# Kernel optimization log

Measured on AMD Instinct MI355X. Metric: run time of the kernel, lower is better.

## Reference

```python
import jax, jax.numpy as jnp
import numpy as np

WS = 8          # window size
DIM = 512       # channels
NH = 16         # heads
HD = DIM // NH  # head dim = 32
N = WS * WS     # tokens per window = 64
NW = 64         # windows per image
B = 16          # images
BW = B * NW     # total windows = 1024
SCALE = HD ** -0.5


def _relative_position_index():
    # Swin relative position index, shape (N, N), values in [0, (2*WS-1)^2)
    coords = np.stack(np.meshgrid(np.arange(WS), np.arange(WS), indexing='ij'))  # (2, WS, WS)
    coords_flat = coords.reshape(2, -1)                                           # (2, N)
    rel = coords_flat[:, :, None] - coords_flat[:, None, :]                       # (2, N, N)
    rel = rel.transpose(1, 2, 0).astype(np.int32)                                 # (N, N, 2)
    rel[:, :, 0] += WS - 1
    rel[:, :, 1] += WS - 1
    rel[:, :, 0] *= 2 * WS - 1
    return jnp.asarray(rel.sum(-1))                                               # (N, N)


def setup_inputs() -> dict:
    key = jax.random.key(0)
    ks = jax.random.split(key, 7)
    x = jax.random.normal(ks[0], (BW, N, DIM), dtype=jnp.float32)
    mask = jax.random.normal(ks[1], (NW, N, N), dtype=jnp.float32)  # shift mask (additive)
    qkv_w = jax.random.normal(ks[2], (3 * DIM, DIM), dtype=jnp.float32) * 0.02
    qkv_b = jax.random.normal(ks[3], (3 * DIM,), dtype=jnp.float32) * 0.02
    rel_bias_table = jax.random.normal(ks[4], ((2 * WS - 1) ** 2, NH), dtype=jnp.float32) * 0.02
    proj_w = jax.random.normal(ks[5], (DIM, DIM), dtype=jnp.float32) * 0.02
    proj_b = jax.random.normal(ks[6], (DIM,), dtype=jnp.float32) * 0.02
    rel_index = _relative_position_index()
    return {"x": x, "mask": mask, "qkv_w": qkv_w, "qkv_b": qkv_b,
            "rel_bias_table": rel_bias_table, "proj_w": proj_w, "proj_b": proj_b,
            "rel_index": rel_index}


def reference(x, mask, qkv_w, qkv_b, rel_bias_table, proj_w, proj_b, rel_index):
    # qkv projection: (BW, N, 3*DIM) -> (3, BW, NH, N, HD)
    qkv = (x @ qkv_w.T + qkv_b).reshape(BW, N, 3, NH, HD).transpose(2, 0, 3, 1, 4)
    q, k, v = qkv[0], qkv[1], qkv[2]
    # scaled dot-product scores: (BW, NH, N, N)
    attn = jnp.einsum('bhnd,bhmd->bhnm', q * SCALE, k)
    # relative position bias: gather (N*N,) -> (N, N, NH) -> (NH, N, N)
    bias = rel_bias_table[rel_index.reshape(-1)].reshape(N, N, NH).transpose(2, 0, 1)
    attn = attn + bias[None]
    # shift mask: broadcast over images and heads
    attn = attn.reshape(B, NW, NH, N, N) + mask[None, :, None]
    attn = jax.nn.softmax(attn.reshape(BW, NH, N, N), axis=-1)
    # weighted values: (BW, NH, N, HD) -> (BW, N, DIM)
    out = jnp.einsum('bhnm,bhmd->bhnd', attn, v).transpose(0, 2, 1, 3).reshape(BW, N, DIM)
    return out @ proj_w.T + proj_b
```

## Files before the change

kernel.cpp:

```cpp
#include <hip/hip_runtime.h>
#include <hip/hip_bf16.h>

typedef __bf16 bf16;
typedef __bf16 bf16x4 __attribute__((ext_vector_type(4)));
typedef __bf16 bf16x8 __attribute__((ext_vector_type(8)));
typedef float  f32x4  __attribute__((ext_vector_type(4)));

#define AS1 __attribute__((address_space(1)))
#define AS3 __attribute__((address_space(3)))

__device__ __forceinline__ void gld_lds16(const void* g, void* l) {
    __builtin_amdgcn_global_load_lds((AS1 void*)g, (AS3 void*)l, 16, 0, 0);
}

__global__ void cvt_kernel(const float* __restrict__ in, bf16* __restrict__ out,
                           int n4) {
    for (long i = (long)blockIdx.x * blockDim.x + threadIdx.x; i < n4;
         i += (long)gridDim.x * blockDim.x) {
        f32x4 v = ((const f32x4*)in)[i];
        bf16x4 h;
#pragma unroll
        for (int e = 0; e < 4; ++e) h[e] = (bf16)v[e];
        ((bf16x4*)out)[i] = h;
    }
}

__global__ void bias_kernel(const int* __restrict__ rel_index,
                            const float* __restrict__ table,
                            float* __restrict__ bias) {
    int idx = blockIdx.x * 256 + threadIdx.x;
    int rc = idx & 4095;
    int h  = idx >> 12;
    bias[idx] = table[rel_index[rc] * 16 + h];
}

#define STAGE(GBASE, LBASE, SK0)                                          \
    { _Pragma("unroll")                                                   \
      for (int c_ = 0; c_ < 2; ++c_)                                      \
          gld_lds16((GBASE) + c_ * 16 * 512 + (SK0),                      \
                    (LBASE) + (w * 2 + c_) * 512); }

#define PHASE(S, KK, IH, LOADB, GB, LB, SK0, VM)                            \
  {                                                                         \
    const bf16* ap_ = sA + ((S)*2+(KK))*8192 + (wm128+(IH)*64+r16)*32 + q*8;\
    _Pragma("unroll")                                                       \
    for (int ii = 0; ii < 4; ++ii) av[ii] = *(const bf16x8*)(ap_ + ii*512); \
    if (LOADB) {                                                            \
      const bf16* bp_ = sB + ((S)*2+(KK))*8192 + (wn64+r16)*32 + q*8;       \
      _Pragma("unroll")                                                     \
      for (int jj = 0; jj < 4; ++jj) bv[jj] = *(const bf16x8*)(bp_+jj*512); \
    }                                                                       \
    STAGE(GB, LB, SK0);                                                     \
    __builtin_amdgcn_sched_barrier(0);                                      \
    __builtin_amdgcn_s_barrier();                                           \
    asm volatile("s_waitcnt lgkmcnt(0)");                                   \
    __builtin_amdgcn_sched_barrier(0);                                      \
    __builtin_amdgcn_s_setprio(1);                                          \
    _Pragma("unroll")                                                       \
    for (int ii = 0; ii < 4; ++ii)                                          \
      _Pragma("unroll")                                                     \
      for (int jj = 0; jj < 4; ++jj)                                        \
        acc[(IH)*4+ii][jj] = __builtin_amdgcn_mfma_f32_16x16x32_bf16(       \
            av[ii], bv[jj], acc[(IH)*4+ii][jj], 0, 0, 0);                   \
    __builtin_amdgcn_s_setprio(0);                                          \
    if (VM) asm volatile("s_waitcnt vmcnt(4)");                             \
    __builtin_amdgcn_sched_barrier(0);                                      \
    __builtin_amdgcn_s_barrier();                                           \
  }

__global__ __launch_bounds__(512, 2) void gemm1_qkv8(
    const bf16* __restrict__ A, const bf16* __restrict__ B,
    const float* __restrict__ bias, bf16* __restrict__ Cq,
    bf16* __restrict__ Ckv)
{
    __shared__ __attribute__((aligned(16))) char smemraw[131072];
    bf16* sA = (bf16*)smemraw;
    bf16* sB = sA + 32768;

    const int t     = threadIdx.x;
    const int w     = t >> 6;
    const int lane  = t & 63;
    const int q     = lane >> 4;
    const int r16   = lane & 15;
    const int wm128 = (w >> 2) * 128;
    const int wn64  = (w & 3) * 64;

    const int bid = blockIdx.x;
    const int wg  = (bid & 7) * 192 + (bid >> 3);
    const long bM = (long)(wg / 6) * 256;
    const long bN = (long)(wg % 6) * 256;

    const bf16* Ast = A + (bM + w * 32 + (lane >> 2)) * 512 + (lane & 3) * 8;
    const bf16* Bst = B + (bN + w * 32 + (lane >> 2)) * 512 + (lane & 3) * 8;

    f32x4 acc[8][4];
#pragma unroll
    for (int i = 0; i < 8; ++i)
#pragma unroll
        for (int j = 0; j < 4; ++j) acc[i][j] = f32x4{0.f, 0.f, 0.f, 0.f};

    bf16x8 av[4], bv[4];

    STAGE(Ast, sA + 0,     0);
    STAGE(Bst, sB + 0,     0);
    STAGE(Ast, sA + 8192,  32);
    STAGE(Bst, sB + 8192,  32);
    STAGE(Ast, sA + 16384, 64);
    STAGE(Bst, sB + 16384, 64);
    asm volatile("s_waitcnt vmcnt(4)");
    __builtin_amdgcn_sched_barrier(0);
    __builtin_amdgcn_s_barrier();

    for (int i = 0; i < 4; ++i) {
        const int t1 = 2 * i + 1;
        const int t2 = (2 * i + 2 < 8) ? 2 * i + 2 : 7;
        const int t3 = (2 * i + 3 < 8) ? 2 * i + 3 : 7;
        PHASE(0, 0, 0, 1, Ast, sA + 24576, t1 * 64 + 32, 0)
        PHASE(0, 0, 1, 0, Bst, sB + 24576, t1 * 64 + 32, 0)
        PHASE(0, 1, 1, 1, Ast, sA + 0,     t2 * 64,      0)
        PHASE(0, 1, 0, 0, Bst, sB + 0,     t2 * 64,      1)
        PHASE(1, 0, 0, 1, Ast, sA + 8192,  t2 * 64 + 32, 0)
        PHASE(1, 0, 1, 0, Bst, sB + 8192,  t2 * 64 + 32, 0)
        PHASE(1, 1, 1, 1, Ast, sA + 16384, t3 * 64,      0)
        PHASE(1, 1, 0, 0, Bst, sB + 16384, t3 * 64,      1)
    }

    asm volatile("s_waitcnt vmcnt(0)");
    __builtin_amdgcn_sched_barrier(0);
    __builtin_amdgcn_s_barrier();

    bf16* ct = (bf16*)smemraw;
#pragma unroll
    for (int j = 0; j < 4; ++j) {
        const int col  = wn64 + j * 16 + r16;
        const float bvv = bias[bN + col];
        const int chunk = col >> 3, cl = col & 7;
#pragma unroll
        for (int i = 0; i < 8; ++i)
#pragma unroll
            for (int r = 0; r < 4; ++r) {
                const int row = wm128 + i * 16 + q * 4 + r;
                ct[row * 256 + ((chunk ^ ((row >> 2) & 7)) << 3) + cl] =
                    (bf16)(acc[i][j][r] + bvv);
            }
    }
    __syncthreads();

    const bool isQ = (bN < 512);
    bf16* __restrict__ outp = isQ ? (Cq + bM * 512 + bN)
                                  : (Ckv + bM * 1024 + (bN - 512));
    const int ostr = isQ ? 512 : 1024;
#pragma unroll
    for (int it = 0; it < 16; ++it) {
        const int row = w * 32 + it * 2 + (lane >> 5);
        const int c   = lane & 31;
        uint4 v = *(const uint4*)(ct + row * 256 +
                                  ((c ^ ((row >> 2) & 7)) << 3));
        *(uint4*)(outp + (long)row * ostr + c * 8) = v;
    }
}

__global__ __launch_bounds__(256) void gemm2_proj(
    const bf16* __restrict__ A, const bf16* __restrict__ B,
    const float* __restrict__ bias, float* __restrict__ C)
{
    __shared__ __attribute__((aligned(16))) bf16 As[128 * 64];
    __shared__ __attribute__((aligned(16))) bf16 Bs[128 * 64];

    const int t    = threadIdx.x;
    const int w    = t >> 6;
    const int lane = t & 63;
    const int q    = lane >> 4;
    const int r16  = lane & 15;
    const int wm   = (w & 1) * 64;
    const int wn   = (w >> 1) * 64;
    const long bM  = (long)blockIdx.x * 128;
    const long bN  = (long)blockIdx.y * 128;

    const int sRow = lane >> 3;
    const int sCol = (lane & 7) * 8;

    f32x4 acc[4][4];
#pragma unroll
    for (int i = 0; i < 4; ++i)
#pragma unroll
        for (int j = 0; j < 4; ++j)
            acc[i][j] = f32x4{0.f, 0.f, 0.f, 0.f};

    for (int k0 = 0; k0 < 512; k0 += 64) {
#pragma unroll
        for (int it = 0; it < 4; ++it) {
            const int chunk = w * 4 + it;
            const int row   = chunk * 8 + sRow;
            gld_lds16(A + (bM + row) * 512L + k0 + sCol, As + chunk * 512);
            gld_lds16(B + (bN + row) * 512L + k0 + sCol, Bs + chunk * 512);
        }
        asm volatile("s_waitcnt vmcnt(0)" ::: "memory");
        __syncthreads();

#pragma unroll
        for (int ks = 0; ks < 2; ++ks) {
            bf16x8 av[4], bv[4];
#pragma unroll
            for (int i = 0; i < 4; ++i)
                av[i] = *(const bf16x8*)&As[(wm + i * 16 + r16) * 64 + ks * 32 + q * 8];
#pragma unroll
            for (int j = 0; j < 4; ++j)
                bv[j] = *(const bf16x8*)&Bs[(wn + j * 16 + r16) * 64 + ks * 32 + q * 8];
#pragma unroll
            for (int i = 0; i < 4; ++i)
#pragma unroll
                for (int j = 0; j < 4; ++j)
                    acc[i][j] = __builtin_amdgcn_mfma_f32_16x16x32_bf16(
                        av[i], bv[j], acc[i][j], 0, 0, 0);
        }
        __syncthreads();
    }

#pragma unroll
    for (int j = 0; j < 4; ++j) {
        const long col = bN + wn + j * 16 + r16;
        const float bvv = bias[col];
#pragma unroll
        for (int i = 0; i < 4; ++i) {
            const long row = bM + wm + i * 16 + q * 4;
#pragma unroll
            for (int r = 0; r < 4; ++r)
                C[(row + r) * 512L + col] = acc[i][j][r] + bvv;
        }
    }
}

__global__ __launch_bounds__(64) void attn_kernel(
    bf16* __restrict__ qbuf, const bf16* __restrict__ kv,
    const float* __restrict__ mask, const float* __restrict__ bias)
{
    __shared__ __attribute__((aligned(16))) bf16 smem[6144];
    bf16* Qs = smem;
    bf16* Ks = smem + 2048;
    bf16* Vt = smem + 4096;
    bf16* Ps = smem;

    const int lane = threadIdx.x;
    const int q    = lane >> 4;
    const int r16  = lane & 15;
    const int bw   = blockIdx.x >> 4;
    const int h    = blockIdx.x & 15;
    const int nw   = bw & 63;
    const long rowbase = (long)bw * 64;

#pragma unroll
    for (int it = 0; it < 4; ++it) {
        const int tok  = it * 16 + (lane >> 2);
        const int part = (lane & 3) * 8;
        gld_lds16(qbuf + (rowbase + tok) * 512  + h * 32 + part, Qs + it * 512);
        gld_lds16(kv   + (rowbase + tok) * 1024 + h * 32 + part, Ks + it * 512);
    }
    {
        const bf16* gv = kv + (rowbase + lane) * 1024 + 512 + h * 32;
        uint4 vtmp[4];
#pragma unroll
        for (int jj = 0; jj < 4; ++jj) vtmp[jj] = ((const uint4*)gv)[jj];
        const bf16* vrow = (const bf16*)vtmp;
#pragma unroll
        for (int hd = 0; hd < 32; ++hd)
            Vt[hd * 64 + lane] = vrow[hd];
    }
    asm volatile("s_waitcnt vmcnt(0)" ::: "memory");
    __syncthreads();

    f32x4 acc[4][4];
    {
        bf16x8 av[4], bv[4];
#pragma unroll
        for (int ti = 0; ti < 4; ++ti)
            av[ti] = *(const bf16x8*)&Qs[(ti * 16 + r16) * 32 + q * 8];
#pragma unroll
        for (int tj = 0; tj < 4; ++tj)
            bv[tj] = *(const bf16x8*)&Ks[(tj * 16 + r16) * 32 + q * 8];
        const f32x4 z = f32x4{0.f, 0.f, 0.f, 0.f};
#pragma unroll
        for (int ti = 0; ti < 4; ++ti)
#pragma unroll
            for (int tj = 0; tj < 4; ++tj)
                acc[ti][tj] = __builtin_amdgcn_mfma_f32_16x16x32_bf16(
                    av[ti], bv[tj], z, 0, 0, 0);
    }

    const float SCALE  = 0.17677669529663687f;
    const float LOG2E  = 1.4426950408889634f;
    const float* biasH = bias + h * 4096;
    const float* maskW = mask + nw * 4096;

#pragma unroll
    for (int ti = 0; ti < 4; ++ti) {
#pragma unroll
        for (int r = 0; r < 4; ++r) {
            const int row = ti * 16 + q * 4 + r;
            float mx = -1e30f;
#pragma unroll
            for (int tj = 0; tj < 4; ++tj) {
                const int col = tj * 16 + r16;
                float s = acc[ti][tj][r] * SCALE
                        + biasH[row * 64 + col] + maskW[row * 64 + col];
                acc[ti][tj][r] = s;
                mx = fmaxf(mx, s);
            }
#pragma unroll
            for (int d = 1; d < 16; d <<= 1)
                mx = fmaxf(mx, __shfl_xor(mx, d, 16));
            float sum = 0.f;
#pragma unroll
            for (int tj = 0; tj < 4; ++tj) {
                float e = exp2f((acc[ti][tj][r] - mx) * LOG2E);
                acc[ti][tj][r] = e;
                sum += e;
            }
#pragma unroll
            for (int d = 1; d < 16; d <<= 1)
                sum += __shfl_xor(sum, d, 16);
            const float inv = 1.0f / sum;
#pragma unroll
            for (int tj = 0; tj < 4; ++tj)
                Ps[row * 64 + tj * 16 + r16] = (bf16)(acc[ti][tj][r] * inv);
        }
    }
    __syncthreads();

    f32x4 o[4][2];
#pragma unroll
    for (int ti = 0; ti < 4; ++ti)
#pragma unroll
        for (int tn = 0; tn < 2; ++tn)
            o[ti][tn] = f32x4{0.f, 0.f, 0.f, 0.f};

#pragma unroll
    for (int ks = 0; ks < 2; ++ks) {
        bf16x8 av[4], bv[2];
#pragma unroll
        for (int ti = 0; ti < 4; ++ti)
            av[ti] = *(const bf16x8*)&Ps[(ti * 16 + r16) * 64 + ks * 32 + q * 8];
#pragma unroll
        for (int tn = 0; tn < 2; ++tn)
            bv[tn] = *(const bf16x8*)&Vt[(tn * 16 + r16) * 64 + ks * 32 + q * 8];
#pragma unroll
        for (int ti = 0; ti < 4; ++ti)
#pragma unroll
            for (int tn = 0; tn < 2; ++tn)
                o[ti][tn] = __builtin_amdgcn_mfma_f32_16x16x32_bf16(
                    av[ti], bv[tn], o[ti][tn], 0, 0, 0);
    }

    bf16* op = qbuf + rowbase * 512 + h * 32;
#pragma unroll
    for (int ti = 0; ti < 4; ++ti)
#pragma unroll
        for (int tn = 0; tn < 2; ++tn)
#pragma unroll
            for (int r = 0; r < 4; ++r)
                op[(long)(ti * 16 + q * 4 + r) * 512 + tn * 16 + r16] =
                    (bf16)(o[ti][tn][r]);
}

extern "C" void kernel_launch(void* const* d_in, const int* in_sizes, int n_in,
                              void* d_out, int out_size, void* d_ws, size_t ws_size,
                              hipStream_t stream) {
    const float* x      = (const float*)d_in[0];
    const float* mask   = (const float*)d_in[1];
    const float* qkv_w  = (const float*)d_in[2];
    const float* qkv_b  = (const float*)d_in[3];
    const float* table  = (const float*)d_in[4];
    const float* proj_w = (const float*)d_in[5];
    const float* proj_b = (const float*)d_in[6];
    const int*   relidx = (const int*)d_in[7];
    float* out = (float*)d_out;

    char*  ws   = (char*)d_ws;
    float* bias = (float*)ws;
    bf16*  qbuf = (bf16*)(ws + 262144);
    bf16*  xbf  = (bf16*)(ws + 67371008);
    bf16*  wq   = (bf16*)(ws + 134479872);
    bf16*  wp   = (bf16*)(ws + 136052736);
    const size_t need_full = 136577024ull + 134217728ull;
    bf16* kvbuf = (ws_size >= need_full) ? (bf16*)(ws + 136577024)
                                         : (bf16*)d_out;

    bias_kernel<<<256, 256, 0, stream>>>(relidx, table, bias);
    cvt_kernel<<<2048, 256, 0, stream>>>(x,      xbf, 8388608);
    cvt_kernel<<<768,  256, 0, stream>>>(qkv_w,  wq,  196608);
    cvt_kernel<<<256,  256, 0, stream>>>(proj_w, wp,  65536);

    gemm1_qkv8<<<1536, 512, 0, stream>>>(xbf, wq, qkv_b, qbuf, kvbuf);
    attn_kernel<<<16384, 64, 0, stream>>>(qbuf, kvbuf, mask, bias);
    gemm2_proj<<<dim3(512, 4), 256, 0, stream>>>(qbuf, wp, proj_b, out);
}
```

Measured before the change: 562.0 us.

## Swizzle LDS layouts, reuse pipelined GEMM for projection, batch four heads per attention block

Adds XOR swizzles to the LDS staging and read addresses in both GEMMs and the attention kernel to cut bank conflicts. The output projection now reuses the 256x256, 8-wave pipelined GEMM body instead of a simple 128x128 kernel, and the softmax scale is folded into the Q projection epilogue. Attention now runs four heads per 256-thread block, with each wave handling one head without block barriers, and writes its output through LDS as coalesced 16-byte stores. Folding the scale before the bf16 rounding of Q slightly changes the numerics, and the projection grid has only 512 large blocks.

```diff
diff --git a/kernel.cpp b/kernel.cpp
--- a/kernel.cpp
+++ b/kernel.cpp
@@ -42,11 +42,11 @@
 
 #define PHASE(S, KK, IH, LOADB, GB, LB, SK0, VM)                            \
   {                                                                         \
-    const bf16* ap_ = sA + ((S)*2+(KK))*8192 + (wm128+(IH)*64+r16)*32 + q*8;\
+    const bf16* ap_ = sA + ((S)*2+(KK))*8192 + (wm128+(IH)*64+r16)*32 + cq8;\
     _Pragma("unroll")                                                       \
     for (int ii = 0; ii < 4; ++ii) av[ii] = *(const bf16x8*)(ap_ + ii*512); \
     if (LOADB) {                                                            \
-      const bf16* bp_ = sB + ((S)*2+(KK))*8192 + (wn64+r16)*32 + q*8;       \
+      const bf16* bp_ = sB + ((S)*2+(KK))*8192 + (wn64+r16)*32 + cq8;       \
       _Pragma("unroll")                                                     \
       for (int jj = 0; jj < 4; ++jj) bv[jj] = *(const bf16x8*)(bp_+jj*512); \
     }                                                                       \
@@ -68,67 +68,70 @@
     __builtin_amdgcn_s_barrier();                                           \
   }
 
+#define GEMM_PREAMBLE                                                       \
+    __shared__ __attribute__((aligned(16))) char smemraw[131072];           \
+    bf16* sA = (bf16*)smemraw;                                              \
+    bf16* sB = sA + 32768;                                                  \
+    const int t     = threadIdx.x;                                          \
+    const int w     = t >> 6;                                               \
+    const int lane  = t & 63;                                               \
+    const int q     = lane >> 4;                                            \
+    const int r16   = lane & 15;                                            \
+    const int wm128 = (w >> 2) * 128;                                       \
+    const int wn64  = (w & 3) * 64;                                         \
+    const int sc8   = (((lane & 3) ^ ((lane >> 2) & 3)) << 3);              \
+    const int cq8   = ((q ^ (r16 & 3)) << 3);
+
+#define GEMM_MAIN(ABASE, BBASE)                                             \
+    const bf16* Ast = (ABASE) + (bM + w * 32 + (lane >> 2)) * 512 + sc8;    \
+    const bf16* Bst = (BBASE) + (bN + w * 32 + (lane >> 2)) * 512 + sc8;    \
+    f32x4 acc[8][4];                                                        \
+    _Pragma("unroll")                                                       \
+    for (int i = 0; i < 8; ++i)                                             \
+        _Pragma("unroll")                                                   \
+        for (int j = 0; j < 4; ++j) acc[i][j] = f32x4{0.f, 0.f, 0.f, 0.f};  \
+    bf16x8 av[4], bv[4];                                                    \
+    STAGE(Ast, sA + 0,     0);                                              \
+    STAGE(Bst, sB + 0,     0);                                              \
+    STAGE(Ast, sA + 8192,  32);                                             \
+    STAGE(Bst, sB + 8192,  32);                                             \
+    STAGE(Ast, sA + 16384, 64);                                             \
+    STAGE(Bst, sB + 16384, 64);                                             \
+    asm volatile("s_waitcnt vmcnt(4)");                                     \
+    __builtin_amdgcn_sched_barrier(0);                                      \
+    __builtin_amdgcn_s_barrier();                                           \
+    for (int i = 0; i < 4; ++i) {                                           \
+        const int t1 = 2 * i + 1;                                           \
+        const int t2 = (2 * i + 2 < 8) ? 2 * i + 2 : 7;                     \
+        const int t3 = (2 * i + 3 < 8) ? 2 * i + 3 : 7;                     \
+        PHASE(0, 0, 0, 1, Ast, sA + 24576, t1 * 64 + 32, 0)                 \
+        PHASE(0, 0, 1, 0, Bst, sB + 24576, t1 * 64 + 32, 0)                 \
+        PHASE(0, 1, 1, 1, Ast, sA + 0,     t2 * 64,      0)                 \
+        PHASE(0, 1, 0, 0, Bst, sB + 0,     t2 * 64,      1)                 \
+        PHASE(1, 0, 0, 1, Ast, sA + 8192,  t2 * 64 + 32, 0)                 \
+        PHASE(1, 0, 1, 0, Bst, sB + 8192,  t2 * 64 + 32, 0)                 \
+        PHASE(1, 1, 1, 1, Ast, sA + 16384, t3 * 64,      0)                 \
+        PHASE(1, 1, 0, 0, Bst, sB + 16384, t3 * 64,      1)                 \
+    }                                                                       \
+    asm volatile("s_waitcnt vmcnt(0)");                                     \
+    __builtin_amdgcn_sched_barrier(0);                                      \
+    __builtin_amdgcn_s_barrier();
+
 __global__ __launch_bounds__(512, 2) void gemm1_qkv8(
     const bf16* __restrict__ A, const bf16* __restrict__ B,
     const float* __restrict__ bias, bf16* __restrict__ Cq,
     bf16* __restrict__ Ckv)
 {
-    __shared__ __attribute__((aligned(16))) char smemraw[131072];
-    bf16* sA = (bf16*)smemraw;
-    bf16* sB = sA + 32768;
-
-    const int t     = threadIdx.x;
-    const int w     = t >> 6;
-    const int lane  = t & 63;
-    const int q     = lane >> 4;
-    const int r16   = lane & 15;
-    const int wm128 = (w >> 2) * 128;
-    const int wn64  = (w & 3) * 64;
-
+    GEMM_PREAMBLE
     const int bid = blockIdx.x;
     const int wg  = (bid & 7) * 192 + (bid >> 3);
     const long bM = (long)(wg / 6) * 256;
     const long bN = (long)(wg % 6) * 256;
 
-    const bf16* Ast = A + (bM + w * 32 + (lane >> 2)) * 512 + (lane & 3) * 8;
-    const bf16* Bst = B + (bN + w * 32 + (lane >> 2)) * 512 + (lane & 3) * 8;
-
-    f32x4 acc[8][4];
-#pragma unroll
-    for (int i = 0; i < 8; ++i)
-#pragma unroll
-        for (int j = 0; j < 4; ++j) acc[i][j] = f32x4{0.f, 0.f, 0.f, 0.f};
-
-    bf16x8 av[4], bv[4];
-
-    STAGE(Ast, sA + 0,     0);
-    STAGE(Bst, sB + 0,     0);
-    STAGE(Ast, sA + 8192,  32);
-    STAGE(Bst, sB + 8192,  32);
-    STAGE(Ast, sA + 16384, 64);
-    STAGE(Bst, sB + 16384, 64);
-    asm volatile("s_waitcnt vmcnt(4)");
-    __builtin_amdgcn_sched_barrier(0);
-    __builtin_amdgcn_s_barrier();
-
-    for (int i = 0; i < 4; ++i) {
-        const int t1 = 2 * i + 1;
-        const int t2 = (2 * i + 2 < 8) ? 2 * i + 2 : 7;
-        const int t3 = (2 * i + 3 < 8) ? 2 * i + 3 : 7;
-        PHASE(0, 0, 0, 1, Ast, sA + 24576, t1 * 64 + 32, 0)
-        PHASE(0, 0, 1, 0, Bst, sB + 24576, t1 * 64 + 32, 0)
-        PHASE(0, 1, 1, 1, Ast, sA + 0,     t2 * 64,      0)
-        PHASE(0, 1, 0, 0, Bst, sB + 0,     t2 * 64,      1)
-        PHASE(1, 0, 0, 1, Ast, sA + 8192,  t2 * 64 + 32, 0)
-        PHASE(1, 0, 1, 0, Bst, sB + 8192,  t2 * 64 + 32, 0)
-        PHASE(1, 1, 1, 1, Ast, sA + 16384, t3 * 64,      0)
-        PHASE(1, 1, 0, 0, Bst, sB + 16384, t3 * 64,      1)
-    }
-
-    asm volatile("s_waitcnt vmcnt(0)");
-    __builtin_amdgcn_sched_barrier(0);
-    __builtin_amdgcn_s_barrier();
-
+    GEMM_MAIN(A, B)
+
+    const bool isQ = (bN < 512);
+    const float sc = isQ ? 0.17677669529663687f : 1.0f;
     bf16* ct = (bf16*)smemraw;
 #pragma unroll
     for (int j = 0; j < 4; ++j) {
@@ -141,12 +144,11 @@
             for (int r = 0; r < 4; ++r) {
                 const int row = wm128 + i * 16 + q * 4 + r;
                 ct[row * 256 + ((chunk ^ ((row >> 2) & 7)) << 3) + cl] =
-                    (bf16)(acc[i][j][r] + bvv);
+                    (bf16)((acc[i][j][r] + bvv) * sc);
             }
     }
     __syncthreads();
 
-    const bool isQ = (bN < 512);
     bf16* __restrict__ outp = isQ ? (Cq + bM * 512 + bN)
                                   : (Ckv + bM * 1024 + (bN - 512));
     const int ostr = isQ ? 512 : 1024;
@@ -160,101 +162,59 @@
     }
 }
 
-__global__ __launch_bounds__(256) void gemm2_proj(
+__global__ __launch_bounds__(512, 2) void gemm2_proj8(
     const bf16* __restrict__ A, const bf16* __restrict__ B,
     const float* __restrict__ bias, float* __restrict__ C)
 {
-    __shared__ __attribute__((aligned(16))) bf16 As[128 * 64];
-    __shared__ __attribute__((aligned(16))) bf16 Bs[128 * 64];
-
+    GEMM_PREAMBLE
+    const int bid = blockIdx.x;
+    const int wg  = (bid & 7) * 64 + (bid >> 3);
+    const long bM = (long)(wg >> 1) * 256;
+    const long bN = (long)(wg & 1) * 256;
+
+    GEMM_MAIN(A, B)
+
+#pragma unroll
+    for (int j = 0; j < 4; ++j) {
+        const long col = bN + wn64 + j * 16 + r16;
+        const float bvv = bias[col];
+#pragma unroll
+        for (int i = 0; i < 8; ++i) {
+            const long row = bM + wm128 + i * 16 + q * 4;
+#pragma unroll
+            for (int r = 0; r < 4; ++r)
+                C[(row + r) * 512L + col] = acc[i][j][r] + bvv;
+        }
+    }
+}
+
+__global__ __launch_bounds__(256) void attn_kernel4(
+    bf16* __restrict__ qbuf, const bf16* __restrict__ kv,
+    const float* __restrict__ mask, const float* __restrict__ bias)
+{
+    __shared__ __attribute__((aligned(16))) bf16 smem[24576];
     const int t    = threadIdx.x;
-    const int w    = t >> 6;
+    const int wv   = t >> 6;
     const int lane = t & 63;
     const int q    = lane >> 4;
     const int r16  = lane & 15;
-    const int wm   = (w & 1) * 64;
-    const int wn   = (w >> 1) * 64;
-    const long bM  = (long)blockIdx.x * 128;
-    const long bN  = (long)blockIdx.y * 128;
-
-    const int sRow = lane >> 3;
-    const int sCol = (lane & 7) * 8;
-
-    f32x4 acc[4][4];
-#pragma unroll
-    for (int i = 0; i < 4; ++i)
-#pragma unroll
-        for (int j = 0; j < 4; ++j)
-            acc[i][j] = f32x4{0.f, 0.f, 0.f, 0.f};
-
-    for (int k0 = 0; k0 < 512; k0 += 64) {
-#pragma unroll
-        for (int it = 0; it < 4; ++it) {
-            const int chunk = w * 4 + it;
-            const int row   = chunk * 8 + sRow;
-            gld_lds16(A + (bM + row) * 512L + k0 + sCol, As + chunk * 512);
-            gld_lds16(B + (bN + row) * 512L + k0 + sCol, Bs + chunk * 512);
-        }
-        asm volatile("s_waitcnt vmcnt(0)" ::: "memory");
-        __syncthreads();
-
-#pragma unroll
-        for (int ks = 0; ks < 2; ++ks) {
-            bf16x8 av[4], bv[4];
-#pragma unroll
-            for (int i = 0; i < 4; ++i)
-                av[i] = *(const bf16x8*)&As[(wm + i * 16 + r16) * 64 + ks * 32 + q * 8];
-#pragma unroll
-            for (int j = 0; j < 4; ++j)
-                bv[j] = *(const bf16x8*)&Bs[(wn + j * 16 + r16) * 64 + ks * 32 + q * 8];
-#pragma unroll
-            for (int i = 0; i < 4; ++i)
-#pragma unroll
-                for (int j = 0; j < 4; ++j)
-                    acc[i][j] = __builtin_amdgcn_mfma_f32_16x16x32_bf16(
-                        av[i], bv[j], acc[i][j], 0, 0, 0);
-        }
-        __syncthreads();
-    }
-
-#pragma unroll
-    for (int j = 0; j < 4; ++j) {
-        const long col = bN + wn + j * 16 + r16;
-        const float bvv = bias[col];
-#pragma unroll
-        for (int i = 0; i < 4; ++i) {
-            const long row = bM + wm + i * 16 + q * 4;
-#pragma unroll
-            for (int r = 0; r < 4; ++r)
-                C[(row + r) * 512L + col] = acc[i][j][r] + bvv;
-        }
-    }
-}
-
-__global__ __launch_bounds__(64) void attn_kernel(
-    bf16* __restrict__ qbuf, const bf16* __restrict__ kv,
-    const float* __restrict__ mask, const float* __restrict__ bias)
-{
-    __shared__ __attribute__((aligned(16))) bf16 smem[6144];
-    bf16* Qs = smem;
-    bf16* Ks = smem + 2048;
-    bf16* Vt = smem + 4096;
-    bf16* Ps = smem;
-
-    const int lane = threadIdx.x;
-    const int q    = lane >> 4;
-    const int r16  = lane & 15;
-    const int bw   = blockIdx.x >> 4;
-    const int h    = blockIdx.x & 15;
+    const int bw   = blockIdx.x >> 2;
+    const int hg   = blockIdx.x & 3;
+    const int h    = hg * 4 + wv;
     const int nw   = bw & 63;
     const long rowbase = (long)bw * 64;
 
+    bf16* Qs = smem + wv * 6144;
+    bf16* Ks = Qs + 2048;
+    bf16* Vt = Qs + 4096;
+    bf16* Ps = Qs;
+
+    const int sc8 = (((lane & 3) ^ ((lane >> 2) & 3)) << 3);
 #pragma unroll
     for (int it = 0; it < 4; ++it) {
-        const int tok  = it * 16 + (lane >> 2);
-        const int part = (lane & 3) * 8;
-        gld_lds16(qbuf + (rowbase + tok) * 512  + h * 32 + part, Qs + it * 512);
-        gld_lds16(kv   + (rowbase + tok) * 1024 + h * 32 + part, Ks + it * 512);
+        const int tok = it * 16 + (lane >> 2);
+        gld_lds16(qbuf + (rowbase + tok) * 512  + h * 32 + sc8, Qs + it * 512);
+        gld_lds16(kv   + (rowbase + tok) * 1024 + h * 32 + sc8, Ks + it * 512);
     }
     {
         const bf16* gv = kv + (rowbase + lane) * 1024 + 512 + h * 32;
@@ -262,22 +222,23 @@
 #pragma unroll
         for (int jj = 0; jj < 4; ++jj) vtmp[jj] = ((const uint4*)gv)[jj];
         const bf16* vrow = (const bf16*)vtmp;
+        const int tchunk = lane >> 3, tin = lane & 7;
 #pragma unroll
         for (int hd = 0; hd < 32; ++hd)
-            Vt[hd * 64 + lane] = vrow[hd];
+            Vt[hd * 64 + ((tchunk ^ (hd & 7)) << 3) + tin] = vrow[hd];
     }
     asm volatile("s_waitcnt vmcnt(0)" ::: "memory");
-    __syncthreads();
-
+
+    const int cq8 = ((q ^ (r16 & 3)) << 3);
     f32x4 acc[4][4];
     {
         bf16x8 av[4], bv[4];
 #pragma unroll
         for (int ti = 0; ti < 4; ++ti)
-            av[ti] = *(const bf16x8*)&Qs[(ti * 16 + r16) * 32 + q * 8];
+            av[ti] = *(const bf16x8*)&Qs[(ti * 16 + r16) * 32 + cq8];
 #pragma unroll
         for (int tj = 0; tj < 4; ++tj)
-            bv[tj] = *(const bf16x8*)&Ks[(tj * 16 + r16) * 32 + q * 8];
+            bv[tj] = *(const bf16x8*)&Ks[(tj * 16 + r16) * 32 + cq8];
         const f32x4 z = f32x4{0.f, 0.f, 0.f, 0.f};
 #pragma unroll
         for (int ti = 0; ti < 4; ++ti)
@@ -287,7 +248,6 @@
                     av[ti], bv[tj], z, 0, 0, 0);
     }
 
-    const float SCALE  = 0.17677669529663687f;
     const float LOG2E  = 1.4426950408889634f;
     const float* biasH = bias + h * 4096;
     const float* maskW = mask + nw * 4096;
@@ -301,7 +261,7 @@
 #pragma unroll
             for (int tj = 0; tj < 4; ++tj) {
                 const int col = tj * 16 + r16;
-                float s = acc[ti][tj][r] * SCALE
+                float s = acc[ti][tj][r]
                         + biasH[row * 64 + col] + maskW[row * 64 + col];
                 acc[ti][tj][r] = s;
                 mx = fmaxf(mx, s);
@@ -321,11 +281,13 @@
                 sum += __shfl_xor(sum, d, 16);
             const float inv = 1.0f / sum;
 #pragma unroll
-            for (int tj = 0; tj < 4; ++tj)
-                Ps[row * 64 + tj * 16 + r16] = (bf16)(acc[ti][tj][r] * inv);
+            for (int tj = 0; tj < 4; ++tj) {
+                const int c = tj * 16 + r16;
+                Ps[row * 64 + ((((c >> 3) ^ (row & 7)) << 3) + (c & 7))] =
+                    (bf16)(acc[ti][tj][r] * inv);
+            }
         }
     }
-    __syncthreads();
 
     f32x4 o[4][2];
 #pragma unroll
@@ -337,12 +299,13 @@
 #pragma unroll
     for (int ks = 0; ks < 2; ++ks) {
         bf16x8 av[4], bv[2];
+        const int ch = (((ks * 4 + q) ^ (r16 & 7)) << 3);
 #pragma unroll
         for (int ti = 0; ti < 4; ++ti)
-            av[ti] = *(const bf16x8*)&Ps[(ti * 16 + r16) * 64 + ks * 32 + q * 8];
+            av[ti] = *(const bf16x8*)&Ps[(ti * 16 + r16) * 64 + ch];
 #pragma unroll
         for (int tn = 0; tn < 2; ++tn)
-            bv[tn] = *(const bf16x8*)&Vt[(tn * 16 + r16) * 64 + ks * 32 + q * 8];
+            bv[tn] = *(const bf16x8*)&Vt[(tn * 16 + r16) * 64 + ch];
 #pragma unroll
         for (int ti = 0; ti < 4; ++ti)
 #pragma unroll
@@ -351,15 +314,26 @@
                     av[ti], bv[tn], o[ti][tn], 0, 0, 0);
     }
 
-    bf16* op = qbuf + rowbase * 512 + h * 32;
 #pragma unroll
     for (int ti = 0; ti < 4; ++ti)
 #pragma unroll
         for (int tn = 0; tn < 2; ++tn)
 #pragma unroll
             for (int r = 0; r < 4; ++r)
-                op[(long)(ti * 16 + q * 4 + r) * 512 + tn * 16 + r16] =
+                Qs[(ti * 16 + q * 4 + r) * 32 + tn * 16 + r16] =
                     (bf16)(o[ti][tn][r]);
+    __syncthreads();
+
+    bf16* op = qbuf + rowbase * 512 + hg * 128;
+#pragma unroll
+    for (int it = 0; it < 4; ++it) {
+        const int idx = it * 256 + t;
+        const int row = idx >> 4;
+        const int c   = idx & 15;
+        const int hl  = c >> 2;
+        uint4 v = *(const uint4*)(smem + hl * 6144 + row * 32 + (c & 3) * 8);
+        *(uint4*)(op + (long)row * 512 + hl * 32 + (c & 3) * 8) = v;
+    }
 }
 
 extern "C" void kernel_launch(void* const* d_in, const int* in_sizes, int n_in,
@@ -391,6 +365,6 @@
     cvt_kernel<<<256,  256, 0, stream>>>(proj_w, wp,  65536);
 
     gemm1_qkv8<<<1536, 512, 0, stream>>>(xbf, wq, qkv_b, qbuf, kvbuf);
-    attn_kernel<<<16384, 64, 0, stream>>>(qbuf, kvbuf, mask, bias);
-    gemm2_proj<<<dim3(512, 4), 256, 0, stream>>>(qbuf, wp, proj_b, out);
-}
+    attn_kernel4<<<4096, 256, 0, stream>>>(qbuf, kvbuf, mask, bias);
+    gemm2_proj8<<<512, 512, 0, stream>>>(qbuf, wp, proj_b, out);
+}
```

New measurement: 534.7 us. 1.05x faster.
